# Performance work log

Hardware: AMD Instinct MI355X
Metric: run time of the kernel (lower is better)

The kernel has to match this reference:

```python
import jax, jax.numpy as jnp
import numpy as np

EMB_DIM = 1024
N_HEADS = 16
HEAD_DIM = EMB_DIM // N_HEADS


def setup_inputs() -> dict:
    key = jax.random.key(0)
    ks = jax.random.split(key, 6)
    B, S, D = 2, 2048, EMB_DIM
    s = 1.0 / np.sqrt(D)
    return {
        "x": jax.random.normal(ks[0], (B, S, D), dtype=jnp.float32),
        "wq": jax.random.normal(ks[1], (D, D), dtype=jnp.float32) * s,
        "wk": jax.random.normal(ks[2], (D, D), dtype=jnp.float32) * s,
        "wv": jax.random.normal(ks[3], (D, D), dtype=jnp.float32) * s,
        "wo": jax.random.normal(ks[4], (D, D), dtype=jnp.float32) * s,
        "bo": jax.random.normal(ks[5], (D,), dtype=jnp.float32) * 0.01,
    }


def reference(x, wq, wk, wv, wo, bo):
    B, S, D = x.shape
    H, Hd = N_HEADS, HEAD_DIM
    # projections (torch Linear: y = x @ W.T; here weights are stored as [in, out])
    q = (x @ wq).reshape(B, S, H, Hd).transpose(0, 2, 1, 3)  # [B,H,S,Hd]
    k = (x @ wk).reshape(B, S, H, Hd).transpose(0, 2, 1, 3)
    v = (x @ wv).reshape(B, S, H, Hd).transpose(0, 2, 1, 3)
    scores = jnp.einsum("bhqd,bhkd->bhqk", q, k)  # [B,H,S,S]
    causal = jnp.tril(jnp.ones((S, S), dtype=bool))  # keep lower triangle
    scores = jnp.where(causal, scores, -jnp.inf)
    weights = jax.nn.softmax(scores / np.sqrt(Hd), axis=-1)
    ctx = jnp.einsum("bhqk,bhkd->bhqd", weights, v)  # [B,H,S,Hd]
    ctx = ctx.transpose(0, 2, 1, 3).reshape(B, S, D)
    return ctx @ wo + bo
```

## Files before the change

kernel.cpp:

```cpp
#include <hip/hip_runtime.h>
#include <hip/hip_bf16.h>

constexpr int B = 2, S = 2048, D = 1024, H = 16, Hd = 64;
constexpr int M = B * S;
constexpr int K = 1024;

typedef __attribute__((ext_vector_type(8))) short short8;
typedef __attribute__((ext_vector_type(4))) float f32x4;

#if __has_builtin(__builtin_amdgcn_exp2f)
#define EXP2F __builtin_amdgcn_exp2f
#else
#define EXP2F exp2f
#endif

__device__ __forceinline__ float bf2f(unsigned short u) {
    return __uint_as_float(((unsigned)u) << 16);
}
__device__ __forceinline__ unsigned short f2bf(float f) {
    unsigned u = __float_as_uint(f);
    u += 0x7FFF + ((u >> 16) & 1);
    return (unsigned short)(u >> 16);
}
__device__ __forceinline__ void gload_lds16(const unsigned short* g, unsigned short* l) {
    __builtin_amdgcn_global_load_lds(
        (const __attribute__((address_space(1))) void*)g,
        (__attribute__((address_space(3))) void*)l, 16, 0, 0);
}

__global__ __launch_bounds__(256) void convert_x_kernel(
    const float* __restrict__ x, unsigned short* __restrict__ xb)
{
    const size_t i = ((size_t)blockIdx.x * 256 + threadIdx.x) * 8;
    float4 a = *(const float4*)(x + i), b = *(const float4*)(x + i + 4);
    ushort4 u0 = {f2bf(a.x), f2bf(a.y), f2bf(a.z), f2bf(a.w)};
    ushort4 u1 = {f2bf(b.x), f2bf(b.y), f2bf(b.z), f2bf(b.w)};
    *(ushort4*)(xb + i) = u0;
    *(ushort4*)(xb + i + 4) = u1;
}

__global__ __launch_bounds__(256) void transpose_w_kernel(
    const float* __restrict__ wq, const float* __restrict__ wk,
    const float* __restrict__ wv, const float* __restrict__ wo,
    unsigned short* __restrict__ wqkv_t, unsigned short* __restrict__ wo_t)
{
    __shared__ float tile[64][65];
    const int z = blockIdx.z;
    const float* w = (z == 0) ? wq : (z == 1) ? wk : (z == 2) ? wv : wo;
    unsigned short* dst = (z == 3) ? wo_t : wqkv_t + (size_t)z * K * K;
    const int k0 = blockIdx.x * 64, n0 = blockIdx.y * 64;
    const int t = threadIdx.x;
    #pragma unroll
    for (int it = 0; it < 16; ++it) {
        int idx = t + it * 256;
        tile[idx >> 6][idx & 63] = w[(size_t)(k0 + (idx >> 6)) * K + n0 + (idx & 63)];
    }
    __syncthreads();
    #pragma unroll
    for (int it = 0; it < 16; ++it) {
        int idx = t + it * 256;
        int r = idx >> 6, c = idx & 63;
        dst[(size_t)(n0 + r) * K + k0 + c] = f2bf(tile[c][r]);
    }
}

__global__ __launch_bounds__(256) void qkv_mfma_kernel(
    const unsigned short* __restrict__ xa, const unsigned short* __restrict__ bt,
    unsigned short* __restrict__ q, unsigned short* __restrict__ k,
    unsigned short* __restrict__ vt)
{
    __shared__ unsigned short A_lds[128][32];
    __shared__ unsigned short B_lds[128][32];
    const int t = threadIdx.x, w = t >> 6, l = t & 63;
    const int lr = l & 15, lg = l >> 4;
    const int wm = w >> 1, wn = w & 1;
    const int m0 = blockIdx.x * 128, n0 = blockIdx.y * 128;
    const int srow = l >> 2, skofs = (l & 3) * 8;

    f32x4 acc[4][4];
    #pragma unroll
    for (int i = 0; i < 4; ++i)
        #pragma unroll
        for (int j = 0; j < 4; ++j) acc[i][j] = (f32x4){0.f, 0.f, 0.f, 0.f};

    for (int k0 = 0; k0 < K; k0 += 32) {
        #pragma unroll
        for (int p = 0; p < 2; ++p) {
            const int c = w * 2 + p;
            gload_lds16(xa + (size_t)(m0 + c * 16 + srow) * K + k0 + skofs, &A_lds[c * 16][0]);
            gload_lds16(bt + (size_t)(n0 + c * 16 + srow) * K + k0 + skofs, &B_lds[c * 16][0]);
        }
        __syncthreads();
        short8 af[4], bf[4];
        #pragma unroll
        for (int i = 0; i < 4; ++i) af[i] = *(const short8*)&A_lds[wm * 64 + i * 16 + lr][lg * 8];
        #pragma unroll
        for (int j = 0; j < 4; ++j) bf[j] = *(const short8*)&B_lds[wn * 64 + j * 16 + lr][lg * 8];
        #pragma unroll
        for (int i = 0; i < 4; ++i)
            #pragma unroll
            for (int j = 0; j < 4; ++j)
                acc[i][j] = __builtin_amdgcn_mfma_f32_16x16x32_bf16(af[i], bf[j], acc[i][j], 0, 0, 0);
        __syncthreads();
    }

    const int z = (n0 >> 10);
    const float scale = (z == 0) ? 0.125f * 1.44269504f : 1.0f;
    #pragma unroll
    for (int i = 0; i < 4; ++i) {
        const int mbase = m0 + wm * 64 + i * 16 + lg * 4;
        #pragma unroll
        for (int j = 0; j < 4; ++j) {
            const int n = n0 + wn * 64 + j * 16 + lr;
            const int nn = n & 1023, hh = nn >> 6, hd = nn & 63;
            #pragma unroll
            for (int r = 0; r < 4; ++r) {
                const int mm = mbase + r, bb = mm >> 11, ss = mm & (S - 1);
                const unsigned short val = f2bf(acc[i][j][r] * scale);
                if (z == 0)      q[((size_t)(bb * H + hh) * S + ss) * Hd + hd] = val;
                else if (z == 1) k[((size_t)(bb * H + hh) * S + ss) * Hd + hd] = val;
                else             vt[((size_t)(bb * H + hh) * Hd + hd) * S + ss] = val;
            }
        }
    }
}

__global__ __launch_bounds__(256) void out_mfma_kernel(
    const unsigned short* __restrict__ a, const unsigned short* __restrict__ bt,
    const float* __restrict__ bias, float* __restrict__ out)
{
    __shared__ unsigned short A_lds[128][32];
    __shared__ unsigned short B_lds[128][32];
    const int t = threadIdx.x, w = t >> 6, l = t & 63;
    const int lr = l & 15, lg = l >> 4;
    const int wm = w >> 1, wn = w & 1;
    const int m0 = blockIdx.x * 128, n0 = blockIdx.y * 128;
    const int srow = l >> 2, skofs = (l & 3) * 8;

    f32x4 acc[4][4];
    #pragma unroll
    for (int i = 0; i < 4; ++i)
        #pragma unroll
        for (int j = 0; j < 4; ++j) acc[i][j] = (f32x4){0.f, 0.f, 0.f, 0.f};

    for (int k0 = 0; k0 < K; k0 += 32) {
        #pragma unroll
        for (int p = 0; p < 2; ++p) {
            const int c = w * 2 + p;
            gload_lds16(a  + (size_t)(m0 + c * 16 + srow) * K + k0 + skofs, &A_lds[c * 16][0]);
            gload_lds16(bt + (size_t)(n0 + c * 16 + srow) * K + k0 + skofs, &B_lds[c * 16][0]);
        }
        __syncthreads();
        short8 af[4], bf[4];
        #pragma unroll
        for (int i = 0; i < 4; ++i) af[i] = *(const short8*)&A_lds[wm * 64 + i * 16 + lr][lg * 8];
        #pragma unroll
        for (int j = 0; j < 4; ++j) bf[j] = *(const short8*)&B_lds[wn * 64 + j * 16 + lr][lg * 8];
        #pragma unroll
        for (int i = 0; i < 4; ++i)
            #pragma unroll
            for (int j = 0; j < 4; ++j)
                acc[i][j] = __builtin_amdgcn_mfma_f32_16x16x32_bf16(af[i], bf[j], acc[i][j], 0, 0, 0);
        __syncthreads();
    }

    #pragma unroll
    for (int i = 0; i < 4; ++i) {
        const int mbase = m0 + wm * 64 + i * 16 + lg * 4;
        #pragma unroll
        for (int j = 0; j < 4; ++j) {
            const int n = n0 + wn * 64 + j * 16 + lr;
            const float bv = bias[n];
            #pragma unroll
            for (int r = 0; r < 4; ++r)
                out[(size_t)(mbase + r) * D + n] = acc[i][j][r] + bv;
        }
    }
}

__global__ __launch_bounds__(256) void attn_mfma_kernel(
    const unsigned short* __restrict__ q, const unsigned short* __restrict__ k,
    const unsigned short* __restrict__ vt, unsigned short* __restrict__ ctx)
{
    __shared__ unsigned short Kb[64 * 64];
    __shared__ unsigned short Vb[64 * 64];
    __shared__ unsigned short P_lds[4][16 * 64];
    const int t = threadIdx.x, w = t >> 6, l = t & 63;
    const int lr = l & 15, lg = l >> 4;

    const int bid = blockIdx.x;
    const int xcd = bid & 7;
    const int j   = bid >> 3;
    const int m   = j >> 5;
    const int c   = j & 31;
    const int bh  = xcd * 4 + m;
    const int bb  = bh >> 4, hh = bh & 15;
    const int qt  = (m & 1) ? (31 - c) : c;

    const int q0 = qt * 64 + w * 16;
    const int diag = qt;
    const size_t base  = (size_t)(bb * H + hh) * S * Hd;
    const size_t vbase = (size_t)(bb * H + hh) * Hd * S;
    const int pswz = (lr & 7) << 3;

    const int srow0 = w * 16 + (l >> 3);
    const int scol  = (l & 7) * 8;

    short8 qf[2];
    #pragma unroll
    for (int cc = 0; cc < 2; ++cc)
        qf[cc] = *(const short8*)(q + base + (size_t)(q0 + lr) * Hd + cc * 32 + lg * 8);

    f32x4 accO[4];
    #pragma unroll
    for (int hb = 0; hb < 4; ++hb) accO[hb] = (f32x4){0.f, 0.f, 0.f, 0.f};
    float l_part = 0.f;

    {
        short8 k0r[2], v0r[2];
        #pragma unroll
        for (int it = 0; it < 2; ++it) {
            const int row = srow0 + it * 8;
            k0r[it] = *(const short8*)(k + base + (size_t)row * Hd + scol);
            v0r[it] = *(const short8*)(vt + vbase + (size_t)row * S + scol);
        }
        #pragma unroll
        for (int it = 0; it < 2; ++it) {
            const int row = srow0 + it * 8;
            const int wc = (scol ^ ((row & 7) * 8));
            *(short8*)&Kb[row * 64 + wc] = k0r[it];
            *(short8*)&Vb[row * 64 + wc] = v0r[it];
        }
    }
    __syncthreads();

    for (int kt = 0; kt <= diag; ++kt) {
        short8 nK[2], nV[2];
        if (kt < diag) {
            const unsigned short* kg = k + base + (size_t)(kt + 1) * 64 * Hd;
            const unsigned short* vg = vt + vbase + (size_t)(kt + 1) * 64;
            #pragma unroll
            for (int it = 0; it < 2; ++it) {
                const int row = srow0 + it * 8;
                nK[it] = *(const short8*)(kg + (size_t)row * Hd + scol);
                nV[it] = *(const short8*)(vg + (size_t)row * S + scol);
            }
        }

        f32x4 accS[4];
        __builtin_amdgcn_s_setprio(1);
        #pragma unroll
        for (int kc = 0; kc < 4; ++kc) {
            accS[kc] = (f32x4){0.f, 0.f, 0.f, 0.f};
            const int krow = kc * 16 + lr;
            #pragma unroll
            for (int cc = 0; cc < 2; ++cc) {
                short8 kf = *(const short8*)&Kb[krow * 64 +
                    ((cc * 32 + lg * 8) ^ ((krow & 7) * 8))];
                accS[kc] = __builtin_amdgcn_mfma_f32_16x16x32_bf16(kf, qf[cc], accS[kc], 0, 0, 0);
            }
        }
        __builtin_amdgcn_s_setprio(0);

        float ps[16];
        if (kt == diag) {
            #pragma unroll
            for (int kc = 0; kc < 4; ++kc)
                #pragma unroll
                for (int r = 0; r < 4; ++r) {
                    float s = accS[kc][r];
                    if (kc * 16 + lg * 4 + r > w * 16 + lr) s = -INFINITY;
                    ps[kc * 4 + r] = EXP2F(s - 16.f);
                }
        } else {
            #pragma unroll
            for (int i = 0; i < 16; ++i)
                ps[i] = EXP2F(accS[i >> 2][i & 3] - 16.f);
        }
        float s8[8];
        #pragma unroll
        for (int i = 0; i < 8; ++i) s8[i] = ps[i] + ps[i + 8];
        l_part += ((s8[0] + s8[4]) + (s8[1] + s8[5])) +
                  ((s8[2] + s8[6]) + (s8[3] + s8[7]));

        #pragma unroll
        for (int kc = 0; kc < 4; ++kc) {
            uint2 pk;
            *(__hip_bfloat162*)&pk.x =
                __float22bfloat162_rn(make_float2(ps[kc * 4 + 0], ps[kc * 4 + 1]));
            *(__hip_bfloat162*)&pk.y =
                __float22bfloat162_rn(make_float2(ps[kc * 4 + 2], ps[kc * 4 + 3]));
            *(uint2*)&P_lds[w][lr * 64 + ((kc * 16 + lg * 4) ^ pswz)] = pk;
        }
        short8 pa[2];
        #pragma unroll
        for (int cc = 0; cc < 2; ++cc)
            pa[cc] = *(const short8*)&P_lds[w][lr * 64 + ((cc * 32 + lg * 8) ^ pswz)];

        __builtin_amdgcn_s_setprio(1);
        #pragma unroll
        for (int hb = 0; hb < 4; ++hb) {
            const int vrow = hb * 16 + lr;
            #pragma unroll
            for (int cc = 0; cc < 2; ++cc) {
                short8 vf = *(const short8*)&Vb[vrow * 64 +
                    ((cc * 32 + lg * 8) ^ ((vrow & 7) * 8))];
                accO[hb] = __builtin_amdgcn_mfma_f32_16x16x32_bf16(vf, pa[cc], accO[hb], 0, 0, 0);
            }
        }
        __builtin_amdgcn_s_setprio(0);

        __syncthreads();
        if (kt < diag) {
            #pragma unroll
            for (int it = 0; it < 2; ++it) {
                const int row = srow0 + it * 8;
                const int wc = (scol ^ ((row & 7) * 8));
                *(short8*)&Kb[row * 64 + wc] = nK[it];
                *(short8*)&Vb[row * 64 + wc] = nV[it];
            }
            __syncthreads();
        }
    }

    float l_run = l_part;
    l_run += __shfl_xor(l_run, 16);
    l_run += __shfl_xor(l_run, 32);
    const float inv = 1.f / l_run;
    unsigned short* crow = ctx + (size_t)(bb * S + q0 + lr) * D + hh * Hd + lg * 4;
    #pragma unroll
    for (int hb = 0; hb < 4; ++hb) {
        ushort4 o;
        o.x = f2bf(accO[hb][0] * inv);
        o.y = f2bf(accO[hb][1] * inv);
        o.z = f2bf(accO[hb][2] * inv);
        o.w = f2bf(accO[hb][3] * inv);
        *(ushort4*)(crow + hb * 16) = o;
    }
}

extern "C" void kernel_launch(void* const* d_in, const int* in_sizes, int n_in,
                              void* d_out, int out_size, void* d_ws, size_t ws_size,
                              hipStream_t stream) {
    const float* x  = (const float*)d_in[0];
    const float* wq = (const float*)d_in[1];
    const float* wk = (const float*)d_in[2];
    const float* wv = (const float*)d_in[3];
    const float* wo = (const float*)d_in[4];
    const float* bo = (const float*)d_in[5];
    float* out = (float*)d_out;

    char* ws = (char*)d_ws;
    unsigned short* x_bf   = (unsigned short*)ws;
    unsigned short* q      = (unsigned short*)(ws + ((size_t)8  << 20));
    unsigned short* kk     = (unsigned short*)(ws + ((size_t)16 << 20));
    unsigned short* vt     = (unsigned short*)(ws + ((size_t)24 << 20));
    unsigned short* ctx    = x_bf;
    unsigned short* wqkv_t = (unsigned short*)(ws + ((size_t)32 << 20));
    unsigned short* wo_t   = (unsigned short*)(ws + ((size_t)38 << 20));

    convert_x_kernel<<<(M * K) / (256 * 8), 256, 0, stream>>>(x, x_bf);
    dim3 gtr(K / 64, K / 64, 4);
    transpose_w_kernel<<<gtr, 256, 0, stream>>>(wq, wk, wv, wo, wqkv_t, wo_t);

    dim3 gqkv(M / 128, 3072 / 128);
    qkv_mfma_kernel<<<gqkv, 256, 0, stream>>>(x_bf, wqkv_t, q, kk, vt);

    attn_mfma_kernel<<<1024, 256, 0, stream>>>(q, kk, vt, ctx);

    dim3 gout(M / 128, D / 128);
    out_mfma_kernel<<<gout, 256, 0, stream>>>(ctx, wo_t, bo, out);
}
```

Measured before the change: 114.2 us.

## Double GEMM K-tile with XOR-swizzled LDS and peel diagonal attention tile

```diff
diff --git a/kernel.cpp b/kernel.cpp
--- a/kernel.cpp
+++ b/kernel.cpp
@@ -69,13 +69,13 @@
     unsigned short* __restrict__ q, unsigned short* __restrict__ k,
     unsigned short* __restrict__ vt)
 {
-    __shared__ unsigned short A_lds[128][32];
-    __shared__ unsigned short B_lds[128][32];
+    __shared__ unsigned short A_lds[128][64];
+    __shared__ unsigned short B_lds[128][64];
     const int t = threadIdx.x, w = t >> 6, l = t & 63;
     const int lr = l & 15, lg = l >> 4;
     const int wm = w >> 1, wn = w & 1;
     const int m0 = blockIdx.x * 128, n0 = blockIdx.y * 128;
-    const int srow = l >> 2, skofs = (l & 3) * 8;
+    const int prow = lr & 7;
 
     f32x4 acc[4][4];
     #pragma unroll
@@ -83,24 +83,32 @@
         #pragma unroll
         for (int j = 0; j < 4; ++j) acc[i][j] = (f32x4){0.f, 0.f, 0.f, 0.f};
 
-    for (int k0 = 0; k0 < K; k0 += 32) {
-        #pragma unroll
-        for (int p = 0; p < 2; ++p) {
-            const int c = w * 2 + p;
-            gload_lds16(xa + (size_t)(m0 + c * 16 + srow) * K + k0 + skofs, &A_lds[c * 16][0]);
-            gload_lds16(bt + (size_t)(n0 + c * 16 + srow) * K + k0 + skofs, &B_lds[c * 16][0]);
-        }
-        __syncthreads();
-        short8 af[4], bf[4];
-        #pragma unroll
-        for (int i = 0; i < 4; ++i) af[i] = *(const short8*)&A_lds[wm * 64 + i * 16 + lr][lg * 8];
-        #pragma unroll
-        for (int j = 0; j < 4; ++j) bf[j] = *(const short8*)&B_lds[wn * 64 + j * 16 + lr][lg * 8];
-        #pragma unroll
-        for (int i = 0; i < 4; ++i)
+    for (int k0 = 0; k0 < K; k0 += 64) {
+        #pragma unroll
+        for (int it = 0; it < 4; ++it) {
+            const int row = w * 32 + it * 8 + (l >> 3);
+            const int scol = ((l & 7) ^ (row & 7)) * 8;
+            gload_lds16(xa + (size_t)(m0 + row) * K + k0 + scol, &A_lds[w * 32 + it * 8][0]);
+            gload_lds16(bt + (size_t)(n0 + row) * K + k0 + scol, &B_lds[w * 32 + it * 8][0]);
+        }
+        __syncthreads();
+        #pragma unroll
+        for (int c = 0; c < 2; ++c) {
+            short8 af[4], bf[4];
+            #pragma unroll
+            for (int i = 0; i < 4; ++i)
+                af[i] = *(const short8*)&A_lds[wm * 64 + i * 16 + lr]
+                        [(c * 32 + lg * 8) ^ (prow * 8)];
             #pragma unroll
             for (int j = 0; j < 4; ++j)
-                acc[i][j] = __builtin_amdgcn_mfma_f32_16x16x32_bf16(af[i], bf[j], acc[i][j], 0, 0, 0);
+                bf[j] = *(const short8*)&B_lds[wn * 64 + j * 16 + lr]
+                        [(c * 32 + lg * 8) ^ (prow * 8)];
+            #pragma unroll
+            for (int i = 0; i < 4; ++i)
+                #pragma unroll
+                for (int j = 0; j < 4; ++j)
+                    acc[i][j] = __builtin_amdgcn_mfma_f32_16x16x32_bf16(af[i], bf[j], acc[i][j], 0, 0, 0);
+        }
         __syncthreads();
     }
 
@@ -129,13 +137,13 @@
     const unsigned short* __restrict__ a, const unsigned short* __restrict__ bt,
     const float* __restrict__ bias, float* __restrict__ out)
 {
-    __shared__ unsigned short A_lds[128][32];
-    __shared__ unsigned short B_lds[128][32];
+    __shared__ unsigned short A_lds[128][64];
+    __shared__ unsigned short B_lds[128][64];
     const int t = threadIdx.x, w = t >> 6, l = t & 63;
     const int lr = l & 15, lg = l >> 4;
     const int wm = w >> 1, wn = w & 1;
     const int m0 = blockIdx.x * 128, n0 = blockIdx.y * 128;
-    const int srow = l >> 2, skofs = (l & 3) * 8;
+    const int prow = lr & 7;
 
     f32x4 acc[4][4];
     #pragma unroll
@@ -143,24 +151,32 @@
         #pragma unroll
         for (int j = 0; j < 4; ++j) acc[i][j] = (f32x4){0.f, 0.f, 0.f, 0.f};
 
-    for (int k0 = 0; k0 < K; k0 += 32) {
-        #pragma unroll
-        for (int p = 0; p < 2; ++p) {
-            const int c = w * 2 + p;
-            gload_lds16(a  + (size_t)(m0 + c * 16 + srow) * K + k0 + skofs, &A_lds[c * 16][0]);
-            gload_lds16(bt + (size_t)(n0 + c * 16 + srow) * K + k0 + skofs, &B_lds[c * 16][0]);
-        }
-        __syncthreads();
-        short8 af[4], bf[4];
-        #pragma unroll
-        for (int i = 0; i < 4; ++i) af[i] = *(const short8*)&A_lds[wm * 64 + i * 16 + lr][lg * 8];
-        #pragma unroll
-        for (int j = 0; j < 4; ++j) bf[j] = *(const short8*)&B_lds[wn * 64 + j * 16 + lr][lg * 8];
-        #pragma unroll
-        for (int i = 0; i < 4; ++i)
+    for (int k0 = 0; k0 < K; k0 += 64) {
+        #pragma unroll
+        for (int it = 0; it < 4; ++it) {
+            const int row = w * 32 + it * 8 + (l >> 3);
+            const int scol = ((l & 7) ^ (row & 7)) * 8;
+            gload_lds16(a  + (size_t)(m0 + row) * K + k0 + scol, &A_lds[w * 32 + it * 8][0]);
+            gload_lds16(bt + (size_t)(n0 + row) * K + k0 + scol, &B_lds[w * 32 + it * 8][0]);
+        }
+        __syncthreads();
+        #pragma unroll
+        for (int c = 0; c < 2; ++c) {
+            short8 af[4], bf[4];
+            #pragma unroll
+            for (int i = 0; i < 4; ++i)
+                af[i] = *(const short8*)&A_lds[wm * 64 + i * 16 + lr]
+                        [(c * 32 + lg * 8) ^ (prow * 8)];
             #pragma unroll
             for (int j = 0; j < 4; ++j)
-                acc[i][j] = __builtin_amdgcn_mfma_f32_16x16x32_bf16(af[i], bf[j], acc[i][j], 0, 0, 0);
+                bf[j] = *(const short8*)&B_lds[wn * 64 + j * 16 + lr]
+                        [(c * 32 + lg * 8) ^ (prow * 8)];
+            #pragma unroll
+            for (int i = 0; i < 4; ++i)
+                #pragma unroll
+                for (int j = 0; j < 4; ++j)
+                    acc[i][j] = __builtin_amdgcn_mfma_f32_16x16x32_bf16(af[i], bf[j], acc[i][j], 0, 0, 0);
+        }
         __syncthreads();
     }
 
@@ -234,9 +250,9 @@
     }
     __syncthreads();
 
-    for (int kt = 0; kt <= diag; ++kt) {
+    for (int kt = 0; kt < diag; ++kt) {
         short8 nK[2], nV[2];
-        if (kt < diag) {
+        {
             const unsigned short* kg = k + base + (size_t)(kt + 1) * 64 * Hd;
             const unsigned short* vg = vt + vbase + (size_t)(kt + 1) * 64;
             #pragma unroll
@@ -263,20 +279,9 @@
         __builtin_amdgcn_s_setprio(0);
 
         float ps[16];
-        if (kt == diag) {
-            #pragma unroll
-            for (int kc = 0; kc < 4; ++kc)
-                #pragma unroll
-                for (int r = 0; r < 4; ++r) {
-                    float s = accS[kc][r];
-                    if (kc * 16 + lg * 4 + r > w * 16 + lr) s = -INFINITY;
-                    ps[kc * 4 + r] = EXP2F(s - 16.f);
-                }
-        } else {
-            #pragma unroll
-            for (int i = 0; i < 16; ++i)
-                ps[i] = EXP2F(accS[i >> 2][i & 3] - 16.f);
-        }
+        #pragma unroll
+        for (int i = 0; i < 16; ++i)
+            ps[i] = EXP2F(accS[i >> 2][i & 3] - 16.f);
         float s8[8];
         #pragma unroll
         for (int i = 0; i < 8; ++i) s8[i] = ps[i] + ps[i + 8];
@@ -311,16 +316,73 @@
         __builtin_amdgcn_s_setprio(0);
 
         __syncthreads();
-        if (kt < diag) {
-            #pragma unroll
-            for (int it = 0; it < 2; ++it) {
-                const int row = srow0 + it * 8;
-                const int wc = (scol ^ ((row & 7) * 8));
-                *(short8*)&Kb[row * 64 + wc] = nK[it];
-                *(short8*)&Vb[row * 64 + wc] = nV[it];
-            }
-            __syncthreads();
-        }
+        #pragma unroll
+        for (int it = 0; it < 2; ++it) {
+            const int row = srow0 + it * 8;
+            const int wc = (scol ^ ((row & 7) * 8));
+            *(short8*)&Kb[row * 64 + wc] = nK[it];
+            *(short8*)&Vb[row * 64 + wc] = nV[it];
+        }
+        __syncthreads();
+    }
+
+    {
+        f32x4 accS[4];
+        __builtin_amdgcn_s_setprio(1);
+        #pragma unroll
+        for (int kc = 0; kc < 4; ++kc) {
+            accS[kc] = (f32x4){0.f, 0.f, 0.f, 0.f};
+            const int krow = kc * 16 + lr;
+            #pragma unroll
+            for (int cc = 0; cc < 2; ++cc) {
+                short8 kf = *(const short8*)&Kb[krow * 64 +
+                    ((cc * 32 + lg * 8) ^ ((krow & 7) * 8))];
+                accS[kc] = __builtin_amdgcn_mfma_f32_16x16x32_bf16(kf, qf[cc], accS[kc], 0, 0, 0);
+            }
+        }
+        __builtin_amdgcn_s_setprio(0);
+
+        float ps[16];
+        #pragma unroll
+        for (int kc = 0; kc < 4; ++kc)
+            #pragma unroll
+            for (int r = 0; r < 4; ++r) {
+                float s = accS[kc][r];
+                if (kc * 16 + lg * 4 + r > w * 16 + lr) s = -INFINITY;
+                ps[kc * 4 + r] = EXP2F(s - 16.f);
+            }
+        float s8[8];
+        #pragma unroll
+        for (int i = 0; i < 8; ++i) s8[i] = ps[i] + ps[i + 8];
+        l_part += ((s8[0] + s8[4]) + (s8[1] + s8[5])) +
+                  ((s8[2] + s8[6]) + (s8[3] + s8[7]));
+
+        #pragma unroll
+        for (int kc = 0; kc < 4; ++kc) {
+            uint2 pk;
+            *(__hip_bfloat162*)&pk.x =
+                __float22bfloat162_rn(make_float2(ps[kc * 4 + 0], ps[kc * 4 + 1]));
+            *(__hip_bfloat162*)&pk.y =
+                __float22bfloat162_rn(make_float2(ps[kc * 4 + 2], ps[kc * 4 + 3]));
+            *(uint2*)&P_lds[w][lr * 64 + ((kc * 16 + lg * 4) ^ pswz)] = pk;
+        }
+        short8 pa[2];
+        #pragma unroll
+        for (int cc = 0; cc < 2; ++cc)
+            pa[cc] = *(const short8*)&P_lds[w][lr * 64 + ((cc * 32 + lg * 8) ^ pswz)];
+
+        __builtin_amdgcn_s_setprio(1);
+        #pragma unroll
+        for (int hb = 0; hb < 4; ++hb) {
+            const int vrow = hb * 16 + lr;
+            #pragma unroll
+            for (int cc = 0; cc < 2; ++cc) {
+                short8 vf = *(const short8*)&Vb[vrow * 64 +
+                    ((cc * 32 + lg * 8) ^ ((vrow & 7) * 8))];
+                accO[hb] = __builtin_amdgcn_mfma_f32_16x16x32_bf16(vf, pa[cc], accO[hb], 0, 0, 0);
+            }
+        }
+        __builtin_amdgcn_s_setprio(0);
     }
 
     float l_run = l_part;
```

Result: slower. 122.7 us (+7.5%).

## Double-buffer K/V tiles in attention and peel causal diagonal iteration

Applied to the files above, without the earlier changes.

```diff
diff --git a/kernel.cpp b/kernel.cpp
--- a/kernel.cpp
+++ b/kernel.cpp
@@ -182,8 +182,8 @@
     const unsigned short* __restrict__ q, const unsigned short* __restrict__ k,
     const unsigned short* __restrict__ vt, unsigned short* __restrict__ ctx)
 {
-    __shared__ unsigned short Kb[64 * 64];
-    __shared__ unsigned short Vb[64 * 64];
+    __shared__ unsigned short Kb[2][64 * 64];
+    __shared__ unsigned short Vb[2][64 * 64];
     __shared__ unsigned short P_lds[4][16 * 64];
     const int t = threadIdx.x, w = t >> 6, l = t & 63;
     const int lr = l & 15, lg = l >> 4;
@@ -192,10 +192,11 @@
     const int xcd = bid & 7;
     const int j   = bid >> 3;
     const int m   = j >> 5;
-    const int c   = j & 31;
+    const int c0  = j & 31;
     const int bh  = xcd * 4 + m;
     const int bb  = bh >> 4, hh = bh & 15;
-    const int qt  = (m & 1) ? (31 - c) : c;
+    const int cc  = (c0 + ((m >> 1) ? 8 : 0)) & 31;
+    const int qt  = (m & 1) ? (31 - cc) : cc;
 
     const int q0 = qt * 64 + w * 16;
     const int diag = qt;
@@ -208,8 +209,8 @@
 
     short8 qf[2];
     #pragma unroll
-    for (int cc = 0; cc < 2; ++cc)
-        qf[cc] = *(const short8*)(q + base + (size_t)(q0 + lr) * Hd + cc * 32 + lg * 8);
+    for (int ci = 0; ci < 2; ++ci)
+        qf[ci] = *(const short8*)(q + base + (size_t)(q0 + lr) * Hd + ci * 32 + lg * 8);
 
     f32x4 accO[4];
     #pragma unroll
@@ -228,15 +229,16 @@
         for (int it = 0; it < 2; ++it) {
             const int row = srow0 + it * 8;
             const int wc = (scol ^ ((row & 7) * 8));
-            *(short8*)&Kb[row * 64 + wc] = k0r[it];
-            *(short8*)&Vb[row * 64 + wc] = v0r[it];
+            *(short8*)&Kb[0][row * 64 + wc] = k0r[it];
+            *(short8*)&Vb[0][row * 64 + wc] = v0r[it];
         }
     }
     __syncthreads();
 
-    for (int kt = 0; kt <= diag; ++kt) {
+    int cur = 0;
+    for (int kt = 0; kt < diag; ++kt) {
         short8 nK[2], nV[2];
-        if (kt < diag) {
+        {
             const unsigned short* kg = k + base + (size_t)(kt + 1) * 64 * Hd;
             const unsigned short* vg = vt + vbase + (size_t)(kt + 1) * 64;
             #pragma unroll
@@ -247,6 +249,9 @@
             }
         }
 
+        const unsigned short* Kc = Kb[cur];
+        const unsigned short* Vc = Vb[cur];
+
         f32x4 accS[4];
         __builtin_amdgcn_s_setprio(1);
         #pragma unroll
@@ -254,29 +259,18 @@
             accS[kc] = (f32x4){0.f, 0.f, 0.f, 0.f};
             const int krow = kc * 16 + lr;
             #pragma unroll
-            for (int cc = 0; cc < 2; ++cc) {
-                short8 kf = *(const short8*)&Kb[krow * 64 +
-                    ((cc * 32 + lg * 8) ^ ((krow & 7) * 8))];
-                accS[kc] = __builtin_amdgcn_mfma_f32_16x16x32_bf16(kf, qf[cc], accS[kc], 0, 0, 0);
+            for (int ci = 0; ci < 2; ++ci) {
+                short8 kf = *(const short8*)&Kc[krow * 64 +
+                    ((ci * 32 + lg * 8) ^ ((krow & 7) * 8))];
+                accS[kc] = __builtin_amdgcn_mfma_f32_16x16x32_bf16(kf, qf[ci], accS[kc], 0, 0, 0);
             }
         }
         __builtin_amdgcn_s_setprio(0);
 
         float ps[16];
-        if (kt == diag) {
-            #pragma unroll
-            for (int kc = 0; kc < 4; ++kc)
-                #pragma unroll
-                for (int r = 0; r < 4; ++r) {
-                    float s = accS[kc][r];
-                    if (kc * 16 + lg * 4 + r > w * 16 + lr) s = -INFINITY;
-                    ps[kc * 4 + r] = EXP2F(s - 16.f);
-                }
-        } else {
-            #pragma unroll
-            for (int i = 0; i < 16; ++i)
-                ps[i] = EXP2F(accS[i >> 2][i & 3] - 16.f);
-        }
+        #pragma unroll
+        for (int i = 0; i < 16; ++i)
+            ps[i] = EXP2F(accS[i >> 2][i & 3] - 16.f);
         float s8[8];
         #pragma unroll
         for (int i = 0; i < 8; ++i) s8[i] = ps[i] + ps[i + 8];
@@ -294,33 +288,92 @@
         }
         short8 pa[2];
         #pragma unroll
-        for (int cc = 0; cc < 2; ++cc)
-            pa[cc] = *(const short8*)&P_lds[w][lr * 64 + ((cc * 32 + lg * 8) ^ pswz)];
+        for (int ci = 0; ci < 2; ++ci)
+            pa[ci] = *(const short8*)&P_lds[w][lr * 64 + ((ci * 32 + lg * 8) ^ pswz)];
 
         __builtin_amdgcn_s_setprio(1);
         #pragma unroll
         for (int hb = 0; hb < 4; ++hb) {
             const int vrow = hb * 16 + lr;
             #pragma unroll
-            for (int cc = 0; cc < 2; ++cc) {
-                short8 vf = *(const short8*)&Vb[vrow * 64 +
-                    ((cc * 32 + lg * 8) ^ ((vrow & 7) * 8))];
-                accO[hb] = __builtin_amdgcn_mfma_f32_16x16x32_bf16(vf, pa[cc], accO[hb], 0, 0, 0);
+            for (int ci = 0; ci < 2; ++ci) {
+                short8 vf = *(const short8*)&Vc[vrow * 64 +
+                    ((ci * 32 + lg * 8) ^ ((vrow & 7) * 8))];
+                accO[hb] = __builtin_amdgcn_mfma_f32_16x16x32_bf16(vf, pa[ci], accO[hb], 0, 0, 0);
             }
         }
         __builtin_amdgcn_s_setprio(0);
 
+        #pragma unroll
+        for (int it = 0; it < 2; ++it) {
+            const int row = srow0 + it * 8;
+            const int wc = (scol ^ ((row & 7) * 8));
+            *(short8*)&Kb[cur ^ 1][row * 64 + wc] = nK[it];
+            *(short8*)&Vb[cur ^ 1][row * 64 + wc] = nV[it];
+        }
         __syncthreads();
-        if (kt < diag) {
-            #pragma unroll
-            for (int it = 0; it < 2; ++it) {
-                const int row = srow0 + it * 8;
-                const int wc = (scol ^ ((row & 7) * 8));
-                *(short8*)&Kb[row * 64 + wc] = nK[it];
-                *(short8*)&Vb[row * 64 + wc] = nV[it];
-            }
-            __syncthreads();
-        }
+        cur ^= 1;
+    }
+
+    {
+        const unsigned short* Kc = Kb[cur];
+        const unsigned short* Vc = Vb[cur];
+        f32x4 accS[4];
+        __builtin_amdgcn_s_setprio(1);
+        #pragma unroll
+        for (int kc = 0; kc < 4; ++kc) {
+            accS[kc] = (f32x4){0.f, 0.f, 0.f, 0.f};
+            const int krow = kc * 16 + lr;
+            #pragma unroll
+            for (int ci = 0; ci < 2; ++ci) {
+                short8 kf = *(const short8*)&Kc[krow * 64 +
+                    ((ci * 32 + lg * 8) ^ ((krow & 7) * 8))];
+                accS[kc] = __builtin_amdgcn_mfma_f32_16x16x32_bf16(kf, qf[ci], accS[kc], 0, 0, 0);
+            }
+        }
+        __builtin_amdgcn_s_setprio(0);
+
+        float ps[16];
+        #pragma unroll
+        for (int kc = 0; kc < 4; ++kc)
+            #pragma unroll
+            for (int r = 0; r < 4; ++r) {
+                float s = accS[kc][r];
+                if (kc * 16 + lg * 4 + r > w * 16 + lr) s = -INFINITY;
+                ps[kc * 4 + r] = EXP2F(s - 16.f);
+            }
+        float s8[8];
+        #pragma unroll
+        for (int i = 0; i < 8; ++i) s8[i] = ps[i] + ps[i + 8];
+        l_part += ((s8[0] + s8[4]) + (s8[1] + s8[5])) +
+                  ((s8[2] + s8[6]) + (s8[3] + s8[7]));
+
+        #pragma unroll
+        for (int kc = 0; kc < 4; ++kc) {
+            uint2 pk;
+            *(__hip_bfloat162*)&pk.x =
+                __float22bfloat162_rn(make_float2(ps[kc * 4 + 0], ps[kc * 4 + 1]));
+            *(__hip_bfloat162*)&pk.y =
+                __float22bfloat162_rn(make_float2(ps[kc * 4 + 2], ps[kc * 4 + 3]));
+            *(uint2*)&P_lds[w][lr * 64 + ((kc * 16 + lg * 4) ^ pswz)] = pk;
+        }
+        short8 pa[2];
+        #pragma unroll
+        for (int ci = 0; ci < 2; ++ci)
+            pa[ci] = *(const short8*)&P_lds[w][lr * 64 + ((ci * 32 + lg * 8) ^ pswz)];
+
+        __builtin_amdgcn_s_setprio(1);
+        #pragma unroll
+        for (int hb = 0; hb < 4; ++hb) {
+            const int vrow = hb * 16 + lr;
+            #pragma unroll
+            for (int ci = 0; ci < 2; ++ci) {
+                short8 vf = *(const short8*)&Vc[vrow * 64 +
+                    ((ci * 32 + lg * 8) ^ ((vrow & 7) * 8))];
+                accO[hb] = __builtin_amdgcn_mfma_f32_16x16x32_bf16(vf, pa[ci], accO[hb], 0, 0, 0);
+            }
+        }
+        __builtin_amdgcn_s_setprio(0);
     }
 
     float l_run = l_part;
```

New measurement: 114.3 us, median of 2. No clear change (+0.1%).
